# Performance work log

Measured on AMD Instinct MI355X. Metric: run time of the kernel, lower is better.

The kernel has to match this reference:

```python
import jax, jax.numpy as jnp
import numpy as np
import math


def _conv2d(x, w, b):
    # 3x3, stride 1, pad 1, NCHW / OIHW
    y = jax.lax.conv_general_dilated(x, w, (1, 1), ((1, 1), (1, 1)),
                                     dimension_numbers=('NCHW', 'OIHW', 'NCHW'))
    return y + b[None, :, None, None]


def _avgpool2(x):
    B, C, H, W = x.shape
    return x.reshape(B, C, H // 2, 2, W // 2, 2).mean(axis=(3, 5))


def setup_inputs() -> dict:
    key = jax.random.key(0)
    ks = jax.random.split(key, 12)
    B, H, W = 8, 512, 512
    x = jax.random.uniform(ks[0], (B, 3, H, W), dtype=jnp.float32)

    def conv_w(k, o, i):
        return jax.random.normal(k, (o, i, 3, 3), jnp.float32) / jnp.sqrt(jnp.float32(i * 9))

    def lin_w(k, o, i):
        return jax.random.normal(k, (o, i), jnp.float32) / jnp.sqrt(jnp.float32(i))

    return {
        'x': x,
        'w1': conv_w(ks[1], 16, 6),  'b1': jnp.zeros((16,), jnp.float32),
        'w2': conv_w(ks[2], 32, 16), 'b2': jnp.zeros((32,), jnp.float32),
        'w3': conv_w(ks[3], 64, 32), 'b3': jnp.zeros((64,), jnp.float32),
        'fw1': lin_w(ks[4], 256, 64),  'fb1': jnp.zeros((256,), jnp.float32),
        'fw2': lin_w(ks[5], 100, 256), 'fb2': jnp.zeros((100,), jnp.float32),
    }


def reference(x, w1, b1, w2, b2, w3, b3, fw1, fb1, fw2, fb2):
    B, C, H, W = x.shape
    # radial distance from image center (torch.meshgrid default = 'ij')
    a, b = jnp.meshgrid(jnp.arange(H), jnp.arange(W), indexing='ij')
    dist = jnp.sqrt((a - H / 2) ** 2 + (b - W / 2) ** 2).astype(jnp.float32)
    max_radius = math.sqrt(H * H + W * W) / 2

    xf = jnp.fft.fftn(x, axes=(-1, -2))
    # torch.fft.fftshift with no dim shifts ALL axes (incl. B, C); jnp matches.
    xf = jnp.fft.fftshift(xf)
    x_mag = jnp.log10(jnp.abs(xf) + 1)

    fi = jnp.concatenate([x, x_mag], axis=1)  # [B,6,H,W]
    y = jax.nn.relu(_conv2d(fi, w1, b1))
    y = _avgpool2(y)
    y = jax.nn.relu(_conv2d(y, w2, b2))
    y = _avgpool2(y)
    y = _conv2d(y, w3, b3)
    y = y.mean(axis=(2, 3))  # AdaptiveAvgPool2d((1,1)) -> [B,64]
    # note: NO activation between the two FC layers in the original
    value_set = jax.nn.leaky_relu((y @ fw1.T + fb1) @ fw2.T + fb2, 0.01)  # [B,100]

    # 100 radial ring bins; replace the 100-iter where-loop with bucketize+gather
    radius_set = max_radius * (jnp.arange(100, dtype=jnp.float32) + 1.0) * 0.01
    # bin i: radius_set[i-1] < dist <= radius_set[i]  ==  searchsorted left
    bin_idx = jnp.clip(jnp.searchsorted(radius_set, dist, side='left'), 0, 99)  # [H,W]
    fq_mask = value_set[:, bin_idx]  # [B,H,W] gather, same math as sum of ring masks

    low = xf * fq_mask[:, None, :, :]
    low = jnp.fft.ifftshift(low)
    low = jnp.fft.ifftn(low, axes=(-1, -2))
    lowpass = jnp.clip(low.real, 0.0, 1.0)
    return lowpass, fq_mask, value_set
```

## Files before the change

### kernel.cpp

```cpp
#include <hip/hip_runtime.h>
#include <math.h>

#define NPIX 262144
#define FSTR 513
#define PPLANE 67080

typedef __attribute__((ext_vector_type(2))) float v2f;


__device__ __forceinline__ int brev9(int i) { return (int)(__brev((unsigned)i) >> 23); }

__device__ __forceinline__ void wave_lds_fence() {
  asm volatile("s_waitcnt lgkmcnt(0)" ::: "memory");
}

__device__ __forceinline__ void gload_lds4(const float* __restrict__ gsrc,
                                           float* __restrict__ ldst) {
  __builtin_amdgcn_global_load_lds(
      (const __attribute__((address_space(1))) void*)gsrc,
      (__attribute__((address_space(3))) void*)ldst, 4, 0, 0);
}

__device__ __forceinline__ void init_tw(float* twr, float* twi, int t) {
  if (t < 256) {
    float ang = -3.14159265358979323846f * (float)t / 256.0f;
    float s, c;
    sincosf(ang, &s, &c);
    twr[t] = c; twi[t] = s;
  }
}

template<bool FWD>
__device__ __forceinline__ void fft512x8(float* __restrict__ sr, float* __restrict__ si,
                                         const float* __restrict__ twr,
                                         const float* __restrict__ twi, int t) {
  const int c  = t >> 5;
  const int tq = t & 31;
  float* cr = sr + c * FSTR;
  float* ci = si + c * FSTR;
  #pragma unroll
  for (int sp = 0; sp < 4; sp++) {
    const int s = 2 * sp;
    const int h = 1 << s;
    if (sp == 0) __syncthreads(); else wave_lds_fence();
    #pragma unroll
    for (int m = 0; m < 4; m++) {
      int q = tq + 32 * m;
      int j = q & (h - 1);
      int base = ((q >> s) << (s + 2)) | j;
      int i1 = j << (8 - s);
      int i2 = j << (7 - s);
      float w1r = twr[i1], w1i = FWD ? twi[i1] : -twi[i1];
      float w2r = twr[i2], w2i = FWD ? twi[i2] : -twi[i2];
      float ar = cr[base],         ai = ci[base];
      float br = cr[base + h],     bi = ci[base + h];
      float c2r = cr[base + 2*h],  c2i = ci[base + 2*h];
      float dr = cr[base + 3*h],   di = ci[base + 3*h];
      float wbr = br * w1r - bi * w1i, wbi = br * w1i + bi * w1r;
      float wdr = dr * w1r - di * w1i, wdi = dr * w1i + di * w1r;
      float t0r = ar + wbr,  t0i = ai + wbi;
      float t1r = ar - wbr,  t1i = ai - wbi;
      float t2r = c2r + wdr, t2i = c2i + wdi;
      float t3r = c2r - wdr, t3i = c2i - wdi;
      float u2r = t2r * w2r - t2i * w2i, u2i = t2r * w2i + t2i * w2r;
      float v3r = t3r * w2r - t3i * w2i, v3i = t3r * w2i + t3i * w2r;
      float u3r = FWD ? v3i : -v3i;
      float u3i = FWD ? -v3r : v3r;
      cr[base]         = t0r + u2r;  ci[base]         = t0i + u2i;
      cr[base + 2*h]   = t0r - u2r;  ci[base + 2*h]   = t0i - u2i;
      cr[base + h]     = t1r + u3r;  ci[base + h]     = t1i + u3i;
      cr[base + 3*h]   = t1r - u3r;  ci[base + 3*h]   = t1i - u3i;
    }
  }
  wave_lds_fence();
  #pragma unroll
  for (int m = 0; m < 8; m++) {
    int k = tq + 32 * m;
    float wr = twr[k], wi = FWD ? twi[k] : -twi[k];
    float vr = cr[k + 256], vi = ci[k + 256];
    float tr = vr * wr - vi * wi;
    float ti = vr * wi + vi * wr;
    float ur = cr[k], ui = ci[k];
    cr[k] = ur + tr;        ci[k] = ui + ti;
    cr[k + 256] = ur - tr;  ci[k + 256] = ui - ti;
  }
  __syncthreads();
}

__device__ __forceinline__ void pair_src(int p, int& ia, int& ib) {
  if (p < 8) { ia = 3 * p; ib = 3 * p + 1; }
  else { int k = p - 8; ia = 6 * k + 2; ib = 6 * k + 5; }
}

__global__ __launch_bounds__(256) void k_fft_rows(const float* __restrict__ x,
                                                  float2* __restrict__ xf) {
  __shared__ float sr[8 * FSTR], si[8 * FSTR], twr[256], twi[256];
  int t = threadIdx.x;
  int p = blockIdx.x >> 6;
  int r0 = (blockIdx.x & 63) << 3;
  init_tw(twr, twi, t);
  int ia, ib;
  pair_src(p, ia, ib);
  const float4* pa = (const float4*)(x + (size_t)ia * NPIX + (size_t)r0 * 512);
  const float4* pb = (const float4*)(x + (size_t)ib * NPIX + (size_t)r0 * 512);
  for (int e = t; e < 1024; e += 256) {
    int row = e >> 7, w = e & 127;
    float4 fa = pa[e];
    float4 fb = pb[e];
    float* cr = sr + row * FSTR;
    float* ci = si + row * FSTR;
    int pc = 4 * w;
    cr[brev9(pc)]     = fa.x;  ci[brev9(pc)]     = fb.x;
    cr[brev9(pc + 1)] = fa.y;  ci[brev9(pc + 1)] = fb.y;
    cr[brev9(pc + 2)] = fa.z;  ci[brev9(pc + 2)] = fb.z;
    cr[brev9(pc + 3)] = fa.w;  ci[brev9(pc + 3)] = fb.w;
  }
  fft512x8<true>(sr, si, twr, twi, t);
  float4* q4 = (float4*)(xf + (size_t)p * NPIX + (size_t)r0 * 512);
  for (int e = t; e < 2048; e += 256) {
    int row = e >> 8, u = e & 255;
    const float* cr = sr + row * FSTR;
    const float* ci = si + row * FSTR;
    q4[e] = make_float4(cr[2 * u], ci[2 * u], cr[2 * u + 1], ci[2 * u + 1]);
  }
}

__global__ __launch_bounds__(256) void k_fft_cols(float2* __restrict__ xf) {
  __shared__ float sr[8 * FSTR], si[8 * FSTR], twr[256], twi[256];
  int t = threadIdx.x;
  int p = blockIdx.x >> 6;
  int c0 = (blockIdx.x & 63) << 3;
  init_tw(twr, twi, t);
  float2* base = xf + (size_t)p * NPIX + c0;
  const int q = t & 3;
  const int j = (t >> 2) & 15;
  const int w = t >> 6;
  #pragma unroll
  for (int it = 0; it < 8; it++) {
    int row = 32 * j + 4 * it + w;
    float4 f = *(const float4*)(base + (size_t)row * 512 + 2 * q);
    int rr = brev9(row);
    sr[(2 * q) * FSTR + rr]     = f.x;  si[(2 * q) * FSTR + rr]     = f.y;
    sr[(2 * q + 1) * FSTR + rr] = f.z;  si[(2 * q + 1) * FSTR + rr] = f.w;
  }
  fft512x8<true>(sr, si, twr, twi, t);
  const int rg = t >> 2;
  #pragma unroll
  for (int it = 0; it < 8; it++) {
    int row = 64 * it + rg;
    float a0 = sr[(2 * q) * FSTR + row],     b0 = si[(2 * q) * FSTR + row];
    float a1 = sr[(2 * q + 1) * FSTR + row], b1 = si[(2 * q + 1) * FSTR + row];
    *(float4*)(base + (size_t)row * 512 + 2 * q) = make_float4(a0, b0, a1, b1);
  }
}

__global__ __launch_bounds__(256) void k_xmag(const float2* __restrict__ xf,
                                              float* __restrict__ xmag) {
  int t = threadIdx.x;
  int p = blockIdx.x >> 6;
  int r0 = (blockIdx.x & 63) << 3;
  int da, db;
  if (p < 8) {
    int bs = (p + 4) & 7;
    da = bs * 3 + 1;
    db = bs * 3 + 2;
  } else {
    int k = p - 8;
    da = ((2 * k + 4) & 7) * 3;
    db = ((2 * k + 5) & 7) * 3;
  }
  const float2* Z = xf + (size_t)p * NPIX;
  float* A = xmag + (size_t)da * NPIX;
  float* B = xmag + (size_t)db * NPIX;
  for (int e = t; e < 2048; e += 256) {
    int row = r0 + (e >> 8);
    int c0 = (e & 255) * 2;
    float4 z01 = *(const float4*)(Z + (size_t)row * 512 + c0);
    int mr = (512 - row) & 511;
    float2 zm0 = Z[(size_t)mr * 512 + ((512 - c0) & 511)];
    float2 zm1 = Z[(size_t)mr * 512 + (511 - c0)];
    float ar0 = 0.5f * (z01.x + zm0.x), ai0 = 0.5f * (z01.y - zm0.y);
    float br0 = 0.5f * (z01.x - zm0.x), bi0 = 0.5f * (z01.y + zm0.y);
    float ar1 = 0.5f * (z01.z + zm1.x), ai1 = 0.5f * (z01.w - zm1.y);
    float br1 = 0.5f * (z01.z - zm1.x), bi1 = 0.5f * (z01.w + zm1.y);
    float ma0 = log10f(sqrtf(ar0 * ar0 + ai0 * ai0) + 1.0f);
    float ma1 = log10f(sqrtf(ar1 * ar1 + ai1 * ai1) + 1.0f);
    float mb0 = log10f(sqrtf(br0 * br0 + bi0 * bi0) + 1.0f);
    float mb1 = log10f(sqrtf(br1 * br1 + bi1 * bi1) + 1.0f);
    size_t off = (size_t)(row ^ 256) * 512 + (c0 ^ 256);
    *(float2*)(A + off) = make_float2(ma0, ma1);
    *(float2*)(B + off) = make_float2(mb0, mb1);
  }
}

__global__ __launch_bounds__(256) void k_conv1(const float* __restrict__ x,
                                               const float* __restrict__ xmag,
                                               const float* __restrict__ w1,
                                               const float* __restrict__ b1,
                                               float* __restrict__ out) {
  __shared__ float tile[2][18 * 132 + 8];
  const int t = threadIdx.x;
  const int tx = t & 31, ty = t >> 5;
  const int bx1 = blockIdx.x, by1 = blockIdx.y;
  const int PC0 = bx1 * 64;
  const int PR0 = by1 * 8;
  const int b  = blockIdx.z >> 1;
  const int og = (blockIdx.z & 1) * 8;
  const int R0 = PR0 * 2 - 1;
  const int C0 = PC0 * 2 - 1;

  if (by1 == 0 || by1 == 31) {
    int row = (by1 == 0) ? 0 : 257;
    int sc = PC0 + 2, len = 64;
    if (bx1 == 0) { sc = 1; len = 65; }
    if (bx1 == 3) { len += 1; }
    #pragma unroll 1
    for (int o = 0; o < 8; o++) {
      float* pl = out + (size_t)(b * 16 + og + o) * PPLANE + (size_t)row * 260;
      for (int e = t; e < len; e += 256) pl[sc + e] = 0.0f;
    }
  }
  if (bx1 == 0 || bx1 == 3) {
    int col = (bx1 == 0) ? 1 : 258;
    if (t < 8) {
      #pragma unroll 1
      for (int o = 0; o < 8; o++) {
        float* pl = out + (size_t)(b * 16 + og + o) * PPLANE + col;
        pl[(size_t)(PR0 + 1 + t) * 260] = 0.0f;
      }
    }
  }

  int li[10], gi[10];
  bool okf[10];
  #pragma unroll
  for (int k = 0; k < 10; k++) {
    int e = t + 256 * k;
    bool valid = e < 2340;
    int i = e / 130, j = e - i * 130;
    int rr = R0 + i, cc = C0 + j;
    bool ok = valid && ((unsigned)rr < 512u) && ((unsigned)cc < 512u);
    li[k] = valid ? (i * 132 + j) : (18 * 132);
    gi[k] = ok ? (rr * 512 + cc) : 0;
    okf[k] = ok;
  }

  v2f acc[8][4];
  #pragma unroll
  for (int o = 0; o < 8; o++)
    #pragma unroll
    for (int q = 0; q < 4; q++) acc[o][q] = (v2f){0.0f, 0.0f};

  const float* xb = x + (size_t)(b * 3) * NPIX;
  const float* mb = xmag + (size_t)(b * 3) * NPIX;

  float ld[10];
  #pragma unroll
  for (int k = 0; k < 10; k++) ld[k] = okf[k] ? xb[gi[k]] : 0.0f;
  #pragma unroll
  for (int k = 0; k < 10; k++) tile[0][li[k]] = ld[k];
  __syncthreads();

  for (int ic = 0; ic < 6; ic++) {
    if (ic < 5) {
      const float* sn = (ic + 1 < 3) ? (xb + (size_t)(ic + 1) * NPIX)
                                     : (mb + (size_t)(ic - 2) * NPIX);
      #pragma unroll
      for (int k = 0; k < 10; k++) ld[k] = okf[k] ? sn[gi[k]] : 0.0f;
    }
    const float* cur = tile[ic & 1];
    float patch[4][6];
    #pragma unroll
    for (int dy = 0; dy < 4; dy++) {
      const float* rp = cur + (2 * ty + dy) * 132 + 4 * tx;
      float4 f = *(const float4*)rp;
      float2 g = *(const float2*)(rp + 4);
      patch[dy][0] = f.x; patch[dy][1] = f.y; patch[dy][2] = f.z;
      patch[dy][3] = f.w; patch[dy][4] = g.x; patch[dy][5] = g.y;
    }
    v2f pr[4][5];
    #pragma unroll
    for (int dy = 0; dy < 4; dy++)
      #pragma unroll
      for (int s = 0; s < 5; s++)
        pr[dy][s] = (v2f){patch[dy][s], patch[dy][s + 1]};
    #pragma unroll
    for (int o = 0; o < 8; o++) {
      const float* wk = w1 + (size_t)((og + o) * 6 + ic) * 9;
      #pragma unroll
      for (int dy = 0; dy < 3; dy++)
        #pragma unroll
        for (int kc = 0; kc < 3; kc++) {
          float kw = wk[dy * 3 + kc];
          v2f wv = (v2f){kw, kw};
          acc[o][0] += wv * pr[dy][kc];
          acc[o][1] += wv * pr[dy][kc + 2];
          acc[o][2] += wv * pr[dy + 1][kc];
          acc[o][3] += wv * pr[dy + 1][kc + 2];
        }
    }
    if (ic < 5) {
      float* nxt = tile[(ic + 1) & 1];
      #pragma unroll
      for (int k = 0; k < 10; k++) nxt[li[k]] = ld[k];
      __syncthreads();
    }
  }
  #pragma unroll
  for (int o = 0; o < 8; o++) {
    float bias = b1[og + o];
    float p0 = fmaxf(acc[o][0].x + bias, 0.0f) + fmaxf(acc[o][0].y + bias, 0.0f)
             + fmaxf(acc[o][2].x + bias, 0.0f) + fmaxf(acc[o][2].y + bias, 0.0f);
    float p1 = fmaxf(acc[o][1].x + bias, 0.0f) + fmaxf(acc[o][1].y + bias, 0.0f)
             + fmaxf(acc[o][3].x + bias, 0.0f) + fmaxf(acc[o][3].y + bias, 0.0f);
    float2* q = (float2*)(out + (size_t)(b * 16 + og + o) * PPLANE
                              + (size_t)(PR0 + ty + 1) * 260 + PC0 + 2 * tx + 2);
    *q = make_float2(p0 * 0.25f, p1 * 0.25f);
  }
}

__global__ __launch_bounds__(256) void k_conv2(const float* __restrict__ in,
                                               const float* __restrict__ w2,
                                               const float* __restrict__ b2,
                                               float* __restrict__ S) {
  __shared__ float tile[2][1216];
  __shared__ float wsum[4][8];
  const int t = threadIdx.x;
  const int tx = t & 31, ty = t >> 5;
  const int bx = blockIdx.x, by = blockIdx.y;
  const int PC0 = bx * 32;
  const int PR0 = by * 8;
  const int b  = blockIdx.z >> 2;
  const int og = (blockIdx.z & 3) * 8;
  const int R0 = PR0 * 2 - 1;
  const int C0 = PC0 * 2 - 1;

  int gi[5];
  #pragma unroll
  for (int k = 0; k < 5; k++) {
    int e = t + 256 * k;
    if (e > 1187) e = 1187;
    int i = e / 66, j = e - 66 * i;
    gi[k] = (R0 + i + 1) * 260 + (C0 + j + 2);
  }

  v2f acc[8][2];
  #pragma unroll
  for (int o = 0; o < 8; o++) {
    acc[o][0] = (v2f){0.0f, 0.0f};
    acc[o][1] = (v2f){0.0f, 0.0f};
  }

  const float* inb = in + (size_t)(b * 16) * PPLANE;
  const int wbase = t & 192;

  auto STAGE = [&](int bsel, int ic) {
    const float* sp = inb + (size_t)ic * PPLANE;
    #pragma unroll
    for (int k = 0; k < 5; k++) {
      if (k < 4 || t < 192)
        gload_lds4(sp + gi[k], &tile[bsel][wbase + 256 * k]);
    }
  };
  auto COMPUTE = [&](int bsel, int ic) {
    const float* cur = tile[bsel];
    float patch[4][4];
    #pragma unroll
    for (int dy = 0; dy < 4; dy++) {
      const float* rp = cur + (2 * ty + dy) * 66 + 2 * tx;
      float2 f0 = *(const float2*)rp;
      float2 f1 = *(const float2*)(rp + 2);
      patch[dy][0] = f0.x; patch[dy][1] = f0.y;
      patch[dy][2] = f1.x; patch[dy][3] = f1.y;
    }
    v2f pr[4][3];
    #pragma unroll
    for (int dy = 0; dy < 4; dy++) {
      pr[dy][0] = (v2f){patch[dy][0], patch[dy][1]};
      pr[dy][1] = (v2f){patch[dy][1], patch[dy][2]};
      pr[dy][2] = (v2f){patch[dy][2], patch[dy][3]};
    }
    #pragma unroll
    for (int o = 0; o < 8; o++) {
      const float* wk = w2 + (size_t)((og + o) * 16 + ic) * 9;
      #pragma unroll
      for (int dy = 0; dy < 3; dy++)
        #pragma unroll
        for (int kc = 0; kc < 3; kc++) {
          float kw = wk[dy * 3 + kc];
          v2f wv = (v2f){kw, kw};
          acc[o][0] += wv * pr[dy][kc];
          acc[o][1] += wv * pr[dy + 1][kc];
        }
    }
  };

  STAGE(0, 0);
  __syncthreads();

  for (int ic = 0; ic < 16; ic++) {
    if (ic < 15) STAGE((ic + 1) & 1, ic + 1);
    COMPUTE(ic & 1, ic);
    if (ic < 15) __syncthreads();
  }

  const int lane = t & 63;
  const int wid = t >> 6;
  float* Sb0 = S + (size_t)(b * 32 + og) * 9;
  #pragma unroll
  for (int o = 0; o < 8; o++) {
    float bias = b2[og + o];
    float v = (fmaxf(acc[o][0].x + bias, 0.0f) + fmaxf(acc[o][0].y + bias, 0.0f)
             + fmaxf(acc[o][1].x + bias, 0.0f) + fmaxf(acc[o][1].y + bias, 0.0f)) * 0.25f;
    float* Sb = Sb0 + o * 9;
    float ts = v;
    #pragma unroll
    for (int off = 32; off > 0; off >>= 1) ts += __shfl_down(ts, off);
    if (lane == 0) wsum[wid][o] = ts;
    if (by == 0) {
      float e = (ty == 0) ? v : 0.0f;
      #pragma unroll
      for (int off = 32; off > 0; off >>= 1) e += __shfl_down(e, off);
      if (lane == 0) atomicAdd(&Sb[1], e);
    }
    if (by == 15) {
      float e = (ty == 7) ? v : 0.0f;
      #pragma unroll
      for (int off = 32; off > 0; off >>= 1) e += __shfl_down(e, off);
      if (lane == 0) atomicAdd(&Sb[2], e);
    }
    if (bx == 0 && tx == 0)  atomicAdd(&Sb[3], v);
    if (bx == 3 && tx == 31) atomicAdd(&Sb[4], v);
    if (bx == 0 && by == 0  && t == 0)   Sb[5] = v;
    if (bx == 3 && by == 0  && t == 31)  Sb[6] = v;
    if (bx == 0 && by == 15 && t == 224) Sb[7] = v;
    if (bx == 3 && by == 15 && t == 255) Sb[8] = v;
  }
  __syncthreads();
  if (t < 8)
    atomicAdd(&Sb0[t * 9], wsum[0][t] + wsum[1][t] + wsum[2][t] + wsum[3][t]);
}

__global__ __launch_bounds__(256) void k_fc(const float* __restrict__ S,
                                            const float* __restrict__ w3,
                                            const float* __restrict__ b3,
                                            const float* __restrict__ fw1,
                                            const float* __restrict__ fb1,
                                            const float* __restrict__ fw2,
                                            const float* __restrict__ fb2,
                                            float* __restrict__ vs_out) {
  __shared__ float Sp[2304];
  __shared__ float y[512];
  __shared__ float h1[2048];
  int t = threadIdx.x;
  for (int e = t; e < 2304; e += 256) {
    int cell = e / 9, k = e - 9 * cell;
    int dy = k / 3, dx = k - 3 * dy;
    const float* s = S + cell * 9;
    float v = s[0];
    if (dy == 0) v -= s[2];
    if (dy == 2) v -= s[1];
    if (dx == 0) v -= s[4];
    if (dx == 2) v -= s[3];
    if (dy == 0 && dx == 0) v += s[8];
    if (dy == 0 && dx == 2) v += s[7];
    if (dy == 2 && dx == 0) v += s[6];
    if (dy == 2 && dx == 2) v += s[5];
    Sp[e] = v;
  }
  __syncthreads();
  for (int e = t; e < 512; e += 256) {
    int b = e >> 6, o = e & 63;
    const float* wrow = w3 + (size_t)o * 288;
    const float* sp = Sp + b * 288;
    float s = 0.0f;
    #pragma unroll 4
    for (int k = 0; k < 288; k++) s += wrow[k] * sp[k];
    y[e] = b3[o] + s * (1.0f / 16384.0f);
  }
  __syncthreads();
  for (int e = t; e < 2048; e += 256) {
    int b = e >> 8, j = e & 255;
    float s = fb1[j];
    for (int k = 0; k < 64; k++) s += y[b * 64 + k] * fw1[j * 64 + k];
    h1[e] = s;
  }
  __syncthreads();
  for (int e = t; e < 800; e += 256) {
    int b = e / 100, i = e - 100 * b;
    float s = fb2[i];
    for (int j = 0; j < 256; j++) s += h1[b * 256 + j] * fw2[i * 256 + j];
    vs_out[e] = (s >= 0.0f) ? s : 0.01f * s;
  }
}

__global__ __launch_bounds__(256) void k_mask(const float* __restrict__ vs,
                                              float* __restrict__ fq_mask) {
  int idx = blockIdx.x * 256 + threadIdx.x;
  int h = idx >> 9, w = idx & 511;
  float da = (float)h - 256.0f, db = (float)w - 256.0f;
  float dist = sqrtf(da * da + db * db);
  int lo = 0, hi = 100;
  while (lo < hi) {
    int mid = (lo + hi) >> 1;
    float r = (362.03867196751236f * (float)(mid + 1)) * 0.01f;
    if (r < dist) lo = mid + 1; else hi = mid;
  }
  int bin = lo > 99 ? 99 : lo;
  #pragma unroll
  for (int b = 0; b < 8; b++)
    fq_mask[(size_t)b * NPIX + idx] = vs[b * 100 + bin];
}

__global__ __launch_bounds__(256) void k_ifft_rows_mod(const float2* __restrict__ xf,
                                                       float2* __restrict__ xf2,
                                                       const float* __restrict__ fq_mask) {
  __shared__ float sr[8 * FSTR], si[8 * FSTR], twr[256], twi[256];
  int t = threadIdx.x;
  int p = blockIdx.x >> 6;
  int r0 = (blockIdx.x & 63) << 3;
  init_tw(twr, twi, t);
  if (p < 8) {
    int bm = (p + 4) & 7;
    const float* mbase = fq_mask + (size_t)bm * NPIX;
    const float4* base4 = (const float4*)(xf + (size_t)p * NPIX + (size_t)r0 * 512);
    for (int e = t; e < 2048; e += 256) {
      int u = (e & 3) | (((e >> 2) & 15) << 3) | (((e >> 6) & 1) << 2) | (((e >> 7) & 1) << 7);
      int row = e >> 8;
      float4 f = base4[row * 256 + u];
      int p0 = 2 * u;
      const float* mrow = mbase + (size_t)((r0 + row + 256) & 511) * 512;
      float2 m = *(const float2*)(mrow + ((p0 + 256) & 511));
      int rr0 = brev9(p0);
      float* cr = sr + row * FSTR;
      float* ci = si + row * FSTR;
      cr[rr0]       = f.x * m.x;  ci[rr0]       = f.y * m.x;
      cr[rr0 + 256] = f.z * m.y;  ci[rr0 + 256] = f.w * m.y;
    }
  } else {
    int k = p - 8;
    const float* fa = fq_mask + (size_t)((2 * k + 4) & 7) * NPIX;
    const float* fb = fq_mask + (size_t)((2 * k + 5) & 7) * NPIX;
    const float2* Z = xf + (size_t)p * NPIX;
    for (int e = t; e < 2048; e += 256) {
      int row = e >> 8;
      int gr = r0 + row;
      int c0 = (e & 255) * 2;
      float4 z01 = *(const float4*)(Z + (size_t)gr * 512 + c0);
      int mr = (512 - gr) & 511;
      float2 zm0 = Z[(size_t)mr * 512 + ((512 - c0) & 511)];
      float2 zm1 = Z[(size_t)mr * 512 + (511 - c0)];
      size_t mro = (size_t)((gr + 256) & 511) * 512;
      int mc = (c0 + 256) & 511;
      float2 ma = *(const float2*)(fa + mro + mc);
      float2 mb = *(const float2*)(fb + mro + mc);
      float s0 = 0.5f * (ma.x + mb.x), d0 = 0.5f * (ma.x - mb.x);
      float s1 = 0.5f * (ma.y + mb.y), d1 = 0.5f * (ma.y - mb.y);
      float wr0 = s0 * z01.x + d0 * zm0.x;
      float wi0 = s0 * z01.y - d0 * zm0.y;
      float wr1 = s1 * z01.z + d1 * zm1.x;
      float wi1 = s1 * z01.w - d1 * zm1.y;
      int rr0 = brev9(c0);
      float* cr = sr + row * FSTR;
      float* ci = si + row * FSTR;
      cr[rr0]       = wr0;  ci[rr0]       = wi0;
      cr[rr0 + 256] = wr1;  ci[rr0 + 256] = wi1;
    }
  }
  fft512x8<false>(sr, si, twr, twi, t);
  float4* o4 = (float4*)(xf2 + (size_t)p * NPIX + (size_t)r0 * 512);
  for (int e = t; e < 2048; e += 256) {
    int row = e >> 8, u = e & 255;
    const float* cr = sr + row * FSTR;
    const float* ci = si + row * FSTR;
    o4[e] = make_float4(cr[2 * u], ci[2 * u], cr[2 * u + 1], ci[2 * u + 1]);
  }
}

__global__ __launch_bounds__(256) void k_ifft_cols_out(const float2* __restrict__ xf2,
                                                       float* __restrict__ lowpass) {
  __shared__ float sr[8 * FSTR], si[8 * FSTR], twr[256], twi[256];
  int t = threadIdx.x;
  int p = blockIdx.x >> 6;
  int c0 = (blockIdx.x & 63) << 3;
  init_tw(twr, twi, t);
  const float2* base = xf2 + (size_t)p * NPIX + c0;
  const int q = t & 3;
  const int j = (t >> 2) & 15;
  const int w = t >> 6;
  #pragma unroll
  for (int it = 0; it < 8; it++) {
    int row = 32 * j + 4 * it + w;
    float4 f = *(const float4*)(base + (size_t)row * 512 + 2 * q);
    int rr = brev9(row);
    sr[(2 * q) * FSTR + rr]     = f.x;  si[(2 * q) * FSTR + rr]     = f.y;
    sr[(2 * q + 1) * FSTR + rr] = f.z;  si[(2 * q + 1) * FSTR + rr] = f.w;
  }
  fft512x8<false>(sr, si, twr, twi, t);
  const float sc = 1.0f / 262144.0f;
  int ia, ib;
  pair_src(p, ia, ib);
  float* oa = lowpass + (size_t)ia * NPIX + c0;
  float* ob = lowpass + (size_t)ib * NPIX + c0;
  const int rg = t >> 2;
  #pragma unroll
  for (int it = 0; it < 8; it++) {
    int row = 64 * it + rg;
    float re0 = sr[(2 * q) * FSTR + row],     im0 = si[(2 * q) * FSTR + row];
    float re1 = sr[(2 * q + 1) * FSTR + row], im1 = si[(2 * q + 1) * FSTR + row];
    float a0 = fminf(fmaxf(re0 * sc, 0.0f), 1.0f);
    float a1 = fminf(fmaxf(re1 * sc, 0.0f), 1.0f);
    float b0 = fminf(fmaxf(im0 * sc, 0.0f), 1.0f);
    float b1 = fminf(fmaxf(im1 * sc, 0.0f), 1.0f);
    *(float2*)(oa + (size_t)row * 512 + 2 * q) = make_float2(a0, a1);
    *(float2*)(ob + (size_t)row * 512 + 2 * q) = make_float2(b0, b1);
  }
}

extern "C" void kernel_launch(void* const* d_in, const int* in_sizes, int n_in,
                              void* d_out, int out_size, void* d_ws, size_t ws_size,
                              hipStream_t stream) {
  const float* x   = (const float*)d_in[0];
  const float* w1  = (const float*)d_in[1];
  const float* b1  = (const float*)d_in[2];
  const float* w2  = (const float*)d_in[3];
  const float* b2  = (const float*)d_in[4];
  const float* w3  = (const float*)d_in[5];
  const float* b3  = (const float*)d_in[6];
  const float* fw1 = (const float*)d_in[7];
  const float* fb1 = (const float*)d_in[8];
  const float* fw2 = (const float*)d_in[9];
  const float* fb2 = (const float*)d_in[10];

  float* lowpass = (float*)d_out;
  float* fq_mask = lowpass + 6291456;
  float* vs      = fq_mask + 2097152;

  float* base    = (float*)d_ws;
  float2* xf     = (float2*)base;
  float* xmag    = base + 6291456;
  float2* xf2    = (float2*)(base + 6291456);
  float* pooled1 = base + 12582912;
  float* S       = pooled1 + 8586240;

  k_fft_rows<<<dim3(12 * 64), 256, 0, stream>>>(x, xf);
  k_fft_cols<<<dim3(12 * 64), 256, 0, stream>>>(xf);
  k_xmag<<<dim3(12 * 64), 256, 0, stream>>>(xf, xmag);

  k_conv1<<<dim3(4, 32, 16), 256, 0, stream>>>(x, xmag, w1, b1, pooled1);
  hipMemsetAsync(S, 0, 2304 * sizeof(float), stream);
  k_conv2<<<dim3(4, 16, 32), 256, 0, stream>>>(pooled1, w2, b2, S);

  k_fc<<<1, 256, 0, stream>>>(S, w3, b3, fw1, fb1, fw2, fb2, vs);
  k_mask<<<1024, 256, 0, stream>>>(vs, fq_mask);

  k_ifft_rows_mod<<<dim3(12 * 64), 256, 0, stream>>>(xf, xf2, fq_mask);
  k_ifft_cols_out<<<dim3(12 * 64), 256, 0, stream>>>(xf2, lowpass);
}
```

Baseline: 361.4 us.

## Read conv2 input directly from global memory instead of LDS double-buffering

The conv2 kernel no longer stages input tiles into LDS with global_load_lds and double buffering. Each thread now loads its overlapping patch rows straight from global memory (float2 loads) and relies on the caches for reuse, which also removes the per-channel barriers. Launch bounds now request 8 blocks per CU to raise occupancy. In exchange, neighbouring threads fetch overlapping data redundantly through L1/L2, and register pressure is constrained by the occupancy hint.

New measurement: 381.8 us. 5.7% more time.

```diff
diff --git a/kernel.cpp b/kernel.cpp
--- a/kernel.cpp
+++ b/kernel.cpp
@@ -12,13 +12,6 @@
 
 __device__ __forceinline__ void wave_lds_fence() {
   asm volatile("s_waitcnt lgkmcnt(0)" ::: "memory");
-}
-
-__device__ __forceinline__ void gload_lds4(const float* __restrict__ gsrc,
-                                           float* __restrict__ ldst) {
-  __builtin_amdgcn_global_load_lds(
-      (const __attribute__((address_space(1))) void*)gsrc,
-      (__attribute__((address_space(3))) void*)ldst, 4, 0, 0);
 }
 
 __device__ __forceinline__ void init_tw(float* twr, float* twi, int t) {
@@ -319,11 +312,10 @@
   }
 }
 
-__global__ __launch_bounds__(256) void k_conv2(const float* __restrict__ in,
-                                               const float* __restrict__ w2,
-                                               const float* __restrict__ b2,
-                                               float* __restrict__ S) {
-  __shared__ float tile[2][1216];
+__global__ __launch_bounds__(256, 8) void k_conv2(const float* __restrict__ in,
+                                                  const float* __restrict__ w2,
+                                                  const float* __restrict__ b2,
+                                                  float* __restrict__ S) {
   __shared__ float wsum[4][8];
   const int t = threadIdx.x;
   const int tx = t & 31, ty = t >> 5;
@@ -332,17 +324,9 @@
   const int PR0 = by * 8;
   const int b  = blockIdx.z >> 2;
   const int og = (blockIdx.z & 3) * 8;
-  const int R0 = PR0 * 2 - 1;
-  const int C0 = PC0 * 2 - 1;
-
-  int gi[5];
-  #pragma unroll
-  for (int k = 0; k < 5; k++) {
-    int e = t + 256 * k;
-    if (e > 1187) e = 1187;
-    int i = e / 66, j = e - 66 * i;
-    gi[k] = (R0 + i + 1) * 260 + (C0 + j + 2);
-  }
+
+  const float* inb = in + (size_t)(b * 16) * PPLANE
+                        + (size_t)(2 * PR0 + 2 * ty) * 260 + (2 * PC0 + 2 * tx);
 
   v2f acc[8][2];
   #pragma unroll
@@ -351,57 +335,38 @@
     acc[o][1] = (v2f){0.0f, 0.0f};
   }
 
-  const float* inb = in + (size_t)(b * 16) * PPLANE;
-  const int wbase = t & 192;
-
-  auto STAGE = [&](int bsel, int ic) {
+  #pragma unroll 1
+  for (int ic = 0; ic < 16; ic++) {
     const float* sp = inb + (size_t)ic * PPLANE;
-    #pragma unroll
-    for (int k = 0; k < 5; k++) {
-      if (k < 4 || t < 192)
-        gload_lds4(sp + gi[k], &tile[bsel][wbase + 256 * k]);
-    }
-  };
-  auto COMPUTE = [&](int bsel, int ic) {
-    const float* cur = tile[bsel];
-    float patch[4][4];
+    const float* wb = w2 + (size_t)(og * 16 + ic) * 9;
     #pragma unroll
     for (int dy = 0; dy < 4; dy++) {
-      const float* rp = cur + (2 * ty + dy) * 66 + 2 * tx;
+      const float* rp = sp + dy * 260;
       float2 f0 = *(const float2*)rp;
       float2 f1 = *(const float2*)(rp + 2);
-      patch[dy][0] = f0.x; patch[dy][1] = f0.y;
-      patch[dy][2] = f1.x; patch[dy][3] = f1.y;
-    }
-    v2f pr[4][3];
-    #pragma unroll
-    for (int dy = 0; dy < 4; dy++) {
-      pr[dy][0] = (v2f){patch[dy][0], patch[dy][1]};
-      pr[dy][1] = (v2f){patch[dy][1], patch[dy][2]};
-      pr[dy][2] = (v2f){patch[dy][2], patch[dy][3]};
-    }
-    #pragma unroll
-    for (int o = 0; o < 8; o++) {
-      const float* wk = w2 + (size_t)((og + o) * 16 + ic) * 9;
-      #pragma unroll
-      for (int dy = 0; dy < 3; dy++)
+      float2 f2 = *(const float2*)(rp + 4);
+      v2f pA = (v2f){f0.y, f1.x};
+      v2f pB = (v2f){f1.x, f1.y};
+      v2f pC = (v2f){f1.y, f2.x};
+      if (dy < 3) {
         #pragma unroll
-        for (int kc = 0; kc < 3; kc++) {
-          float kw = wk[dy * 3 + kc];
-          v2f wv = (v2f){kw, kw};
-          acc[o][0] += wv * pr[dy][kc];
-          acc[o][1] += wv * pr[dy + 1][kc];
+        for (int o = 0; o < 8; o++) {
+          const float* wk = wb + (size_t)o * 144 + 3 * dy;
+          acc[o][0] += (v2f){wk[0], wk[0]} * pA
+                     + (v2f){wk[1], wk[1]} * pB
+                     + (v2f){wk[2], wk[2]} * pC;
         }
-    }
-  };
-
-  STAGE(0, 0);
-  __syncthreads();
-
-  for (int ic = 0; ic < 16; ic++) {
-    if (ic < 15) STAGE((ic + 1) & 1, ic + 1);
-    COMPUTE(ic & 1, ic);
-    if (ic < 15) __syncthreads();
+      }
+      if (dy >= 1) {
+        #pragma unroll
+        for (int o = 0; o < 8; o++) {
+          const float* wk = wb + (size_t)o * 144 + 3 * (dy - 1);
+          acc[o][1] += (v2f){wk[0], wk[0]} * pA
+                     + (v2f){wk[1], wk[1]} * pB
+                     + (v2f){wk[2], wk[2]} * pC;
+        }
+      }
+    }
   }
 
   const int lane = t & 63;
```
